# Kernel tuning notes

Hardware: AMD Instinct MI355X
Metric: run time of the kernel (lower is better)

Reference implementation:

```python
import jax, jax.numpy as jnp
import numpy as np

N_SOTU, N_TAXON, N_EDGES, H = 100000, 50000, 1000000, 128

def setup_inputs() -> dict:
    key = jax.random.key(0)
    ks = jax.random.split(key, 8)
    return {
        "z_sotu": jax.random.normal(ks[0], (N_SOTU, H), dtype=jnp.float32),
        "z_taxon": jax.random.normal(ks[1], (N_TAXON, H), dtype=jnp.float32),
        "row": jax.random.randint(ks[2], (N_EDGES,), 0, N_SOTU, dtype=jnp.int64),
        "col": jax.random.randint(ks[3], (N_EDGES,), 0, N_TAXON, dtype=jnp.int64),
        "w1": jax.random.normal(ks[4], (H, 2 * H), dtype=jnp.float32) * 0.05,
        "b1": jax.random.normal(ks[5], (H,), dtype=jnp.float32) * 0.05,
        "w2": jax.random.normal(ks[6], (1, H), dtype=jnp.float32) * 0.05,
        "b2": jax.random.normal(ks[7], (1,), dtype=jnp.float32) * 0.05,
    }

def reference(z_sotu, z_taxon, row, col, w1, b1, w2, b2):
    # Gather edge endpoints and concat: [E, 2H]
    z = jnp.concatenate([z_sotu[row], z_taxon[col]], axis=-1)
    # 2-layer MLP (torch Linear: y = x @ W.T + b)
    h = jax.nn.relu(jnp.einsum('eh,oh->eo', z, w1) + b1)
    out = jnp.einsum('eh,oh->eo', h, w2) + b2
    return out.reshape(-1)
```

## Files before the change

kernel.cpp:

```cpp
#include <hip/hip_runtime.h>
#include <hip/hip_bf16.h>


#define HID  128
#define FTE  128

typedef __attribute__((ext_vector_type(8)))  short    bf16x8;
typedef __attribute__((ext_vector_type(16))) float    f32x16;
typedef __attribute__((ext_vector_type(4)))  unsigned uint4v;

__device__ __forceinline__ float bf2f(unsigned short u) {
    return __uint_as_float(((unsigned)u) << 16);
}
__device__ __forceinline__ unsigned pk2(float x, float y) {
    __hip_bfloat162 t = __float22bfloat162_rn(make_float2(x, y));
    return *reinterpret_cast<unsigned*>(&t);
}
__device__ __forceinline__ bf16x8 pack8(float4 a, float4 b) {
    uint4v r;
    r.x = pk2(a.x, a.y); r.y = pk2(a.z, a.w);
    r.z = pk2(b.x, b.y); r.w = pk2(b.z, b.w);
    return *reinterpret_cast<bf16x8*>(&r);
}

__global__ __launch_bounds__(256)
void prep_kernel(const float* __restrict__ zs, const float* __restrict__ zt,
                 const float* __restrict__ w1, const float* __restrict__ b1,
                 unsigned short* __restrict__ U, unsigned short* __restrict__ V,
                 int NS, int NT, int NBU)
{
    const bool isU = (int)blockIdx.x < NBU;
    const float* z      = isU ? zs : zt;
    unsigned short* O   = isU ? U  : V;
    const int N    = isU ? NS : NT;
    const int s0   = (isU ? blockIdx.x : blockIdx.x - NBU) * 128;
    const int koff = isU ? 0 : 128;

    const int tid  = threadIdx.x;
    const int wave = tid >> 6;
    const int lane = tid & 63;
    const int l31  = lane & 31;
    const int hlf  = lane >> 5;

    bf16x8 afrag[8];
    {
        const float* wrow = w1 + (32 * wave + l31) * 256 + koff + hlf * 8;
        #pragma unroll
        for (int ks = 0; ks < 8; ++ks) {
            const float4 a = *(const float4*)(wrow + ks * 16);
            const float4 b = *(const float4*)(wrow + ks * 16 + 4);
            afrag[ks] = pack8(a, b);
        }
    }

    f32x16 acc[4] = {};
    #pragma unroll
    for (int ks = 0; ks < 8; ++ks) {
        #pragma unroll
        for (int nt = 0; nt < 4; ++nt) {
            int s = s0 + 32 * nt + l31;
            if (s >= N) s = N - 1;
            const float* src = z + s * HID + ks * 16 + hlf * 8;
            const float4 a = *(const float4*)(src);
            const float4 b = *(const float4*)(src + 4);
            const bf16x8 bfrag = pack8(a, b);
            acc[nt] = __builtin_amdgcn_mfma_f32_32x32x16_bf16(afrag[ks], bfrag, acc[nt], 0, 0, 0);
        }
    }

    float b1v[16];
    #pragma unroll
    for (int g = 0; g < 4; ++g) {
        const int hb = 32 * wave + 8 * g + 4 * hlf;
        if (isU) {
            const float4 bb = *(const float4*)(b1 + hb);
            b1v[4*g+0] = bb.x; b1v[4*g+1] = bb.y; b1v[4*g+2] = bb.z; b1v[4*g+3] = bb.w;
        } else {
            b1v[4*g+0] = b1v[4*g+1] = b1v[4*g+2] = b1v[4*g+3] = 0.0f;
        }
    }

    #pragma unroll
    for (int nt = 0; nt < 4; ++nt) {
        const int s = s0 + 32 * nt + l31;
        if (s < N) {
            #pragma unroll
            for (int g = 0; g < 4; ++g) {
                const int cb = 32 * wave + 8 * g + 4 * hlf;
                uint2 o;
                o.x = pk2(acc[nt][4*g+0] + b1v[4*g+0], acc[nt][4*g+1] + b1v[4*g+1]);
                o.y = pk2(acc[nt][4*g+2] + b1v[4*g+2], acc[nt][4*g+3] + b1v[4*g+3]);
                *(uint2*)(O + s * HID + cb) = o;
            }
        }
    }
}

__global__ __launch_bounds__(256)
void edge_kernel(const unsigned short* __restrict__ U,
                 const unsigned short* __restrict__ V,
                 const int*   __restrict__ row, const int* __restrict__ col,
                 const float* __restrict__ w2, const float* __restrict__ b2,
                 float* __restrict__ out, int E)
{
    const int tid = threadIdx.x;
    const int g   = tid >> 4;
    const int c16 = tid & 15;

    const long long eb = (long long)blockIdx.x * 32 + g * 2;
    const long long e0 = eb, e1 = eb + 1;
    const long long ec0 = e0 < E ? e0 : E - 1;
    const long long ec1 = e1 < E ? e1 : E - 1;

    const int r0 = row[ec0], c0 = col[ec0];
    const int r1 = row[ec1], c1 = col[ec1];
    const bf16x8 u0 = *(const bf16x8*)(U + r0 * HID + c16 * 8);
    const bf16x8 v0 = *(const bf16x8*)(V + c0 * HID + c16 * 8);
    const bf16x8 u1 = *(const bf16x8*)(U + r1 * HID + c16 * 8);
    const bf16x8 v1 = *(const bf16x8*)(V + c1 * HID + c16 * 8);

    const float4 wa = *(const float4*)(w2 + c16 * 8);
    const float4 wb = *(const float4*)(w2 + c16 * 8 + 4);
    float w2v[8] = {wa.x, wa.y, wa.z, wa.w, wb.x, wb.y, wb.z, wb.w};

    float p0 = 0.0f, p1 = 0.0f;
    #pragma unroll
    for (int j = 0; j < 8; ++j) {
        const float h0 = fmaxf(bf2f((unsigned short)u0[j]) + bf2f((unsigned short)v0[j]), 0.0f);
        const float h1 = fmaxf(bf2f((unsigned short)u1[j]) + bf2f((unsigned short)v1[j]), 0.0f);
        p0 = fmaf(h0, w2v[j], p0);
        p1 = fmaf(h1, w2v[j], p1);
    }
    #pragma unroll
    for (int d = 1; d < 16; d <<= 1) {
        p0 += __shfl_xor(p0, d, 64);
        p1 += __shfl_xor(p1, d, 64);
    }
    if (c16 == 0) {
        const float bb = b2[0];
        if (e0 < E) out[e0] = p0 + bb;
        if (e1 < E) out[e1] = p1 + bb;
    }
}

__global__ __launch_bounds__(256, 2)
void edge_mlp_fused(const float* __restrict__ z_sotu, const float* __restrict__ z_taxon,
                    const int* __restrict__ row, const int* __restrict__ col,
                    const float* __restrict__ w1, const float* __restrict__ b1,
                    const float* __restrict__ w2, const float* __restrict__ b2,
                    float* __restrict__ out, int E)
{
    __shared__ __align__(16) unsigned short zsh[FTE * 256];
    const int tid  = threadIdx.x;
    const int wave = tid >> 6;
    const int lane = tid & 63;
    const int l31  = lane & 31;
    const int hlf  = lane >> 5;
    const long long e0 = (long long)blockIdx.x * FTE;
    {
        const int ch  = lane & 15;
        const int rhl = lane >> 4;
        #pragma unroll
        for (int pass = 0; pass < 16; ++pass) {
            const int rh = pass * 4 + rhl;
            const int r  = 32 * wave + (rh >> 1);
            const int hh = rh & 1;
            long long e = e0 + r;
            if (e >= E) e = E - 1;
            const int idx = hh ? col[e] : row[e];
            const float* src = (hh ? z_taxon : z_sotu) + (long long)idx * HID + ch * 8;
            const float4 a = *(const float4*)(src);
            const float4 b = *(const float4*)(src + 4);
            const int c = hh * 16 + ch;
            const int q = c ^ (r & 31);
            *(bf16x8*)(zsh + r * 256 + q * 8) = pack8(a, b);
        }
    }
    bf16x8 afrag[16];
    {
        const float* wrow = w1 + (32 * wave + l31) * 256 + hlf * 8;
        #pragma unroll
        for (int ks = 0; ks < 16; ++ks) {
            const float4 a = *(const float4*)(wrow + ks * 16);
            const float4 b = *(const float4*)(wrow + ks * 16 + 4);
            afrag[ks] = pack8(a, b);
        }
    }
    __syncthreads();
    f32x16 acc[4] = {};
    #pragma unroll
    for (int ks = 0; ks < 16; ++ks) {
        #pragma unroll
        for (int nt = 0; nt < 4; ++nt) {
            const int el = 32 * nt + l31;
            const int q  = (2 * ks + hlf) ^ l31;
            bf16x8 bfrag = *(const bf16x8*)(zsh + el * 256 + q * 8);
            acc[nt] = __builtin_amdgcn_mfma_f32_32x32x16_bf16(afrag[ks], bfrag, acc[nt], 0, 0, 0);
        }
    }
    __syncthreads();
    float* partial = (float*)zsh;
    float b1v[16], w2v[16];
    #pragma unroll
    for (int g = 0; g < 4; ++g) {
        const int hb = 32 * wave + 8 * g + 4 * hlf;
        const float4 bb = *(const float4*)(b1 + hb);
        const float4 ww = *(const float4*)(w2 + hb);
        b1v[4*g+0] = bb.x; b1v[4*g+1] = bb.y; b1v[4*g+2] = bb.z; b1v[4*g+3] = bb.w;
        w2v[4*g+0] = ww.x; w2v[4*g+1] = ww.y; w2v[4*g+2] = ww.z; w2v[4*g+3] = ww.w;
    }
    #pragma unroll
    for (int nt = 0; nt < 4; ++nt) {
        float p = 0.0f;
        #pragma unroll
        for (int r = 0; r < 16; ++r) {
            const float h = fmaxf(acc[nt][r] + b1v[r], 0.0f);
            p = fmaf(h, w2v[r], p);
        }
        p += __shfl_xor(p, 32, 64);
        if (hlf == 0)
            partial[wave * FTE + 32 * nt + l31] = p;
    }
    __syncthreads();
    if (tid < FTE) {
        const long long e = e0 + tid;
        if (e < E) {
            out[e] = partial[0 * FTE + tid] + partial[1 * FTE + tid]
                   + partial[2 * FTE + tid] + partial[3 * FTE + tid]
                   + b2[0];
        }
    }
}

extern "C" void kernel_launch(void* const* d_in, const int* in_sizes, int n_in,
                              void* d_out, int out_size, void* d_ws, size_t ws_size,
                              hipStream_t stream) {
    const float* z_sotu  = (const float*)d_in[0];
    const float* z_taxon = (const float*)d_in[1];
    const int*   row     = (const int*)d_in[2];
    const int*   col     = (const int*)d_in[3];
    const float* w1      = (const float*)d_in[4];
    const float* b1      = (const float*)d_in[5];
    const float* w2      = (const float*)d_in[6];
    const float* b2      = (const float*)d_in[7];
    float*       out     = (float*)d_out;

    const int NS = in_sizes[0] / HID;
    const int NT = in_sizes[1] / HID;
    const int E  = in_sizes[2];
    const size_t need = ((size_t)NS + NT) * HID * 2;

    if (ws_size >= need) {
        unsigned short* U = (unsigned short*)d_ws;
        unsigned short* Vv = U + (size_t)NS * HID;
        const int NBU = (NS + 127) / 128;
        const int NBV = (NT + 127) / 128;
        hipLaunchKernelGGL(prep_kernel, dim3(NBU + NBV), dim3(256), 0, stream,
                           z_sotu, z_taxon, w1, b1, U, Vv, NS, NT, NBU);
        const int nblocks = (E + 31) / 32;
        hipLaunchKernelGGL(edge_kernel, dim3(nblocks), dim3(256), 0, stream,
                           U, Vv, row, col, w2, b2, out, E);
    } else {
        const int nblocks = (E + FTE - 1) / FTE;
        hipLaunchKernelGGL(edge_mlp_fused, dim3(nblocks), dim3(256), 0, stream,
                           z_sotu, z_taxon, row, col, w1, b1, w2, b2, out, E);
    }
}
```

Before: 227.1 us.

## Stage prep tiles in padded LDS and process four edges per group

The prep kernel now loads each 128-row fp32 tile once with coalesced reads, converts it to bf16 into a padded shared-memory buffer, and feeds the MFMA loop from LDS. Before, each wave re-read strided global memory for every k-step. The edge kernel now handles four edges per 16-lane group instead of two, which raises memory-level parallelism for the gathers and allows one vectorized float4 output store. The cost is more LDS use and a barrier in prep, plus higher register pressure and fewer blocks in the edge kernel.

Measured after the change: 203.6 us. -10.3%, faster.

```diff
diff --git a/kernel.cpp b/kernel.cpp
--- a/kernel.cpp
+++ b/kernel.cpp
@@ -4,6 +4,7 @@
 
 #define HID  128
 #define FTE  128
+#define PST  136
 
 typedef __attribute__((ext_vector_type(8)))  short    bf16x8;
 typedef __attribute__((ext_vector_type(16))) float    f32x16;
@@ -29,6 +30,8 @@
                  unsigned short* __restrict__ U, unsigned short* __restrict__ V,
                  int NS, int NT, int NBU)
 {
+    __shared__ __align__(16) unsigned short zl[128 * PST];
+
     const bool isU = (int)blockIdx.x < NBU;
     const float* z      = isU ? zs : zt;
     unsigned short* O   = isU ? U  : V;
@@ -42,6 +45,19 @@
     const int l31  = lane & 31;
     const int hlf  = lane >> 5;
 
+    #pragma unroll
+    for (int i = 0; i < 8; ++i) {
+        const int f = i * 256 + tid;
+        const int r = f >> 4;
+        const int c = f & 15;
+        int s = s0 + r;
+        if (s >= N) s = N - 1;
+        const float* src = z + (long long)s * HID + c * 8;
+        const float4 a = *(const float4*)(src);
+        const float4 b = *(const float4*)(src + 4);
+        *(bf16x8*)(zl + r * PST + c * 8) = pack8(a, b);
+    }
+
     bf16x8 afrag[8];
     {
         const float* wrow = w1 + (32 * wave + l31) * 256 + koff + hlf * 8;
@@ -52,18 +68,15 @@
             afrag[ks] = pack8(a, b);
         }
     }
+    __syncthreads();
 
     f32x16 acc[4] = {};
     #pragma unroll
     for (int ks = 0; ks < 8; ++ks) {
         #pragma unroll
         for (int nt = 0; nt < 4; ++nt) {
-            int s = s0 + 32 * nt + l31;
-            if (s >= N) s = N - 1;
-            const float* src = z + s * HID + ks * 16 + hlf * 8;
-            const float4 a = *(const float4*)(src);
-            const float4 b = *(const float4*)(src + 4);
-            const bf16x8 bfrag = pack8(a, b);
+            const int el = 32 * nt + l31;
+            const bf16x8 bfrag = *(const bf16x8*)(zl + el * PST + (2 * ks + hlf) * 8);
             acc[nt] = __builtin_amdgcn_mfma_f32_32x32x16_bf16(afrag[ks], bfrag, acc[nt], 0, 0, 0);
         }
     }
@@ -90,7 +103,7 @@
                 uint2 o;
                 o.x = pk2(acc[nt][4*g+0] + b1v[4*g+0], acc[nt][4*g+1] + b1v[4*g+1]);
                 o.y = pk2(acc[nt][4*g+2] + b1v[4*g+2], acc[nt][4*g+3] + b1v[4*g+3]);
-                *(uint2*)(O + s * HID + cb) = o;
+                *(uint2*)(O + (long long)s * HID + cb) = o;
             }
         }
     }
@@ -107,39 +120,50 @@
     const int g   = tid >> 4;
     const int c16 = tid & 15;
 
-    const long long eb = (long long)blockIdx.x * 32 + g * 2;
-    const long long e0 = eb, e1 = eb + 1;
-    const long long ec0 = e0 < E ? e0 : E - 1;
-    const long long ec1 = e1 < E ? e1 : E - 1;
-
-    const int r0 = row[ec0], c0 = col[ec0];
-    const int r1 = row[ec1], c1 = col[ec1];
-    const bf16x8 u0 = *(const bf16x8*)(U + r0 * HID + c16 * 8);
-    const bf16x8 v0 = *(const bf16x8*)(V + c0 * HID + c16 * 8);
-    const bf16x8 u1 = *(const bf16x8*)(U + r1 * HID + c16 * 8);
-    const bf16x8 v1 = *(const bf16x8*)(V + c1 * HID + c16 * 8);
+    const long long eb = (long long)blockIdx.x * 64 + g * 4;
+
+    int ri[4], ci[4];
+    #pragma unroll
+    for (int j = 0; j < 4; ++j) {
+        long long e = eb + j;
+        if (e >= E) e = E - 1;
+        ri[j] = row[e]; ci[j] = col[e];
+    }
+    bf16x8 u[4], v[4];
+    #pragma unroll
+    for (int j = 0; j < 4; ++j) {
+        u[j] = *(const bf16x8*)(U + (long long)ri[j] * HID + c16 * 8);
+        v[j] = *(const bf16x8*)(V + (long long)ci[j] * HID + c16 * 8);
+    }
 
     const float4 wa = *(const float4*)(w2 + c16 * 8);
     const float4 wb = *(const float4*)(w2 + c16 * 8 + 4);
-    float w2v[8] = {wa.x, wa.y, wa.z, wa.w, wb.x, wb.y, wb.z, wb.w};
-
-    float p0 = 0.0f, p1 = 0.0f;
-    #pragma unroll
-    for (int j = 0; j < 8; ++j) {
-        const float h0 = fmaxf(bf2f((unsigned short)u0[j]) + bf2f((unsigned short)v0[j]), 0.0f);
-        const float h1 = fmaxf(bf2f((unsigned short)u1[j]) + bf2f((unsigned short)v1[j]), 0.0f);
-        p0 = fmaf(h0, w2v[j], p0);
-        p1 = fmaf(h1, w2v[j], p1);
+    const float w2v[8] = {wa.x, wa.y, wa.z, wa.w, wb.x, wb.y, wb.z, wb.w};
+
+    float p[4] = {0.0f, 0.0f, 0.0f, 0.0f};
+    #pragma unroll
+    for (int j = 0; j < 4; ++j) {
+        #pragma unroll
+        for (int k = 0; k < 8; ++k) {
+            const float h = fmaxf(bf2f((unsigned short)u[j][k]) +
+                                  bf2f((unsigned short)v[j][k]), 0.0f);
+            p[j] = fmaf(h, w2v[k], p[j]);
+        }
     }
     #pragma unroll
     for (int d = 1; d < 16; d <<= 1) {
-        p0 += __shfl_xor(p0, d, 64);
-        p1 += __shfl_xor(p1, d, 64);
+        #pragma unroll
+        for (int j = 0; j < 4; ++j) p[j] += __shfl_xor(p[j], d, 64);
     }
     if (c16 == 0) {
         const float bb = b2[0];
-        if (e0 < E) out[e0] = p0 + bb;
-        if (e1 < E) out[e1] = p1 + bb;
+        if (eb + 3 < E) {
+            *(float4*)(out + eb) = make_float4(p[0] + bb, p[1] + bb, p[2] + bb, p[3] + bb);
+        } else {
+            #pragma unroll
+            for (int j = 0; j < 4; ++j)
+                if (eb + j < E) out[eb + j] = p[j] + bb;
+        }
     }
 }
 
@@ -257,7 +281,7 @@
         const int NBV = (NT + 127) / 128;
         hipLaunchKernelGGL(prep_kernel, dim3(NBU + NBV), dim3(256), 0, stream,
                            z_sotu, z_taxon, w1, b1, U, Vv, NS, NT, NBU);
-        const int nblocks = (E + 31) / 32;
+        const int nblocks = (E + 63) / 64;
         hipLaunchKernelGGL(edge_kernel, dim3(nblocks), dim3(256), 0, stream,
                            U, Vv, row, col, w2, b2, out, E);
     } else {
```
